# Performance work log

Measured on AMD Instinct MI355X. Metric: run time of the kernel, lower is better.

## Reference

```python
import jax, jax.numpy as jnp
import numpy as np

EPS = 1e-12
N = 8192
D_LOW = 2


def setup_inputs() -> dict:
    key = jax.random.key(0)
    k1, k2 = jax.random.split(key)
    # High-dim affinity distribution: strictly positive, sums to 1 (t-SNE P matrix)
    u = jax.random.uniform(k1, (N, N), dtype=jnp.float32, minval=0.1, maxval=1.0)
    P = u / u.sum()
    # Learned low-dim embedding (nn.Embedding(n, d).weight)
    Y = jax.random.normal(k2, (N, D_LOW), dtype=jnp.float32)
    dof = 1  # Student-t degrees of freedom (standard t-SNE)
    return {"P": P, "Y": Y, "dof": dof}


def reference(P, Y, dof):
    # Pairwise squared Euclidean distances: D[i,j] = ||Y_i - Y_j||^2
    Y2 = jnp.sum(Y * Y, axis=1, keepdims=True)          # (n, 1)
    Dm = Y2 - 2.0 * (Y @ Y.T) + Y2.T                     # (n, n)
    # Student-t affinities with zeroed diagonal
    Q = (1.0 + Dm / dof) ** (-(dof + 1) / 2.0)
    Q = Q.at[jnp.diag_indices(Q.shape[0])].set(0.0)
    # Global normalization + clamp
    Q = jnp.clip(Q / jnp.sum(Q), EPS)
    # KL(P || Q)  (metric == 'kl' branch)
    return jnp.sum(P * jnp.log(P / Q))
```

## Files before the change

kernel.cpp:

```cpp
#include <hip/hip_runtime.h>


static constexpr int NROWS = 8192;

__global__ __launch_bounds__(256) void kl_partial_kernel(
    const float* __restrict__ P, const float* __restrict__ Y,
    double* __restrict__ ws)
{
    const int nquads = (NROWS / 4) * NROWS;
    int tid = blockIdx.x * blockDim.x + threadIdx.x;
    int stride = gridDim.x * blockDim.x;

    const float4* __restrict__ P4 = reinterpret_cast<const float4*>(P);
    const float4* __restrict__ Y4 = reinterpret_cast<const float4*>(Y);
    const float2* __restrict__ Y2 = reinterpret_cast<const float2*>(Y);
    const float LOG_EPS = -27.63102111592855f;

    double sA = 0.0, sB = 0.0, sS = 0.0, sC = 0.0;

    for (int f = tid; f < nquads; f += stride) {
        int i  = f >> 11;
        int jq = f & 2047;
        int j0 = jq << 2;

        float4 p  = P4[f];
        float2 yi = Y2[i];
        float4 ya = Y4[jq << 1];
        float4 yb = Y4[(jq << 1) + 1];

        float pv[4]  = {p.x,  p.y,  p.z,  p.w};
        float yjx[4] = {ya.x, ya.z, yb.x, yb.z};
        float yjy[4] = {ya.y, ya.w, yb.y, yb.w};

#pragma unroll
        for (int k = 0; k < 4; ++k) {
            float dx  = yi.x - yjx[k];
            float dy  = yi.y - yjy[k];
            float opd = 1.0f + (dx * dx + dy * dy);
            if ((j0 + k) == i) {
                sC += (double)(pv[k] * (__logf(pv[k]) - LOG_EPS));
            } else {
                sS += (double)(1.0f / opd);
                sA += (double)(pv[k] * __logf(pv[k] * opd));
                sB += (double)pv[k];
            }
        }
    }

#pragma unroll
    for (int off = 32; off > 0; off >>= 1) {
        sA += __shfl_down(sA, off);
        sB += __shfl_down(sB, off);
        sS += __shfl_down(sS, off);
        sC += __shfl_down(sC, off);
    }

    __shared__ double red[4][4];
    int wave = threadIdx.x >> 6;
    int lane = threadIdx.x & 63;
    if (lane == 0) {
        red[wave][0] = sA; red[wave][1] = sB;
        red[wave][2] = sS; red[wave][3] = sC;
    }
    __syncthreads();
    if (threadIdx.x == 0) {
        double a = 0.0, b = 0.0, s = 0.0, c = 0.0;
#pragma unroll
        for (int w = 0; w < 4; ++w) {
            a += red[w][0]; b += red[w][1]; s += red[w][2]; c += red[w][3];
        }
        atomicAdd(&ws[0], a);
        atomicAdd(&ws[1], b);
        atomicAdd(&ws[2], s);
        atomicAdd(&ws[3], c);
    }
}

__global__ void kl_final_kernel(const double* __restrict__ ws,
                                float* __restrict__ out)
{
    double A = ws[0], B = ws[1], S = ws[2], C = ws[3];
    out[0] = (float)(A + B * log(S) + C);
}

extern "C" void kernel_launch(void* const* d_in, const int* in_sizes, int n_in,
                              void* d_out, int out_size, void* d_ws, size_t ws_size,
                              hipStream_t stream) {
    const float* P = (const float*)d_in[0];
    const float* Y = (const float*)d_in[1];
    double* ws = (double*)d_ws;

    hipMemsetAsync(d_ws, 0, 4 * sizeof(double), stream);

    dim3 grid(2048), block(256);
    hipLaunchKernelGGL(kl_partial_kernel, grid, block, 0, stream, P, Y, ws);
    hipLaunchKernelGGL(kl_final_kernel, dim3(1), dim3(1), 0, stream,
                       ws, (float*)d_out);
}
```

Measured before the change: 432.1 us.

## Map one block per row, use float accumulators, correct diagonal in final kernel

New measurement: 589.9 us. 36.5% more time.

```diff
diff --git a/kernel.cpp b/kernel.cpp
--- a/kernel.cpp
+++ b/kernel.cpp
@@ -1,86 +1,105 @@
 #include <hip/hip_runtime.h>
 
 
-static constexpr int NROWS = 8192;
+static constexpr int N_PTS = 8192;
+static constexpr int TPB   = 256;
+static constexpr int QPR   = N_PTS / 4;
+static constexpr int ITER  = QPR / TPB;
 
-__global__ __launch_bounds__(256) void kl_partial_kernel(
+__global__ __launch_bounds__(TPB) void kl_partial_kernel(
     const float* __restrict__ P, const float* __restrict__ Y,
     double* __restrict__ ws)
 {
-    const int nquads = (NROWS / 4) * NROWS;
-    int tid = blockIdx.x * blockDim.x + threadIdx.x;
-    int stride = gridDim.x * blockDim.x;
+    const int row = blockIdx.x;
+    const int t   = threadIdx.x;
+    const float4* __restrict__ P4 =
+        reinterpret_cast<const float4*>(P) + (size_t)row * QPR;
+    const float4* __restrict__ Y4 = reinterpret_cast<const float4*>(Y);
 
-    const float4* __restrict__ P4 = reinterpret_cast<const float4*>(P);
-    const float4* __restrict__ Y4 = reinterpret_cast<const float4*>(Y);
-    const float2* __restrict__ Y2 = reinterpret_cast<const float2*>(Y);
-    const float LOG_EPS = -27.63102111592855f;
+    const float yix = Y[2 * row];
+    const float yiy = Y[2 * row + 1];
 
-    double sA = 0.0, sB = 0.0, sS = 0.0, sC = 0.0;
+    float sA0 = 0.f, sA1 = 0.f, sB0 = 0.f, sB1 = 0.f, sS0 = 0.f, sS1 = 0.f;
 
-    for (int f = tid; f < nquads; f += stride) {
-        int i  = f >> 11;
-        int jq = f & 2047;
-        int j0 = jq << 2;
+#pragma unroll
+    for (int it = 0; it < ITER; ++it) {
+        const int jq = t + it * TPB;
+        float4 p  = P4[jq];
+        float4 ya = Y4[2 * jq];
+        float4 yb = Y4[2 * jq + 1];
 
-        float4 p  = P4[f];
-        float2 yi = Y2[i];
-        float4 ya = Y4[jq << 1];
-        float4 yb = Y4[(jq << 1) + 1];
-
-        float pv[4]  = {p.x,  p.y,  p.z,  p.w};
-        float yjx[4] = {ya.x, ya.z, yb.x, yb.z};
-        float yjy[4] = {ya.y, ya.w, yb.y, yb.w};
+        float pv[4] = {p.x,  p.y,  p.z,  p.w};
+        float jx[4] = {ya.x, ya.z, yb.x, yb.z};
+        float jy[4] = {ya.y, ya.w, yb.y, yb.w};
 
 #pragma unroll
         for (int k = 0; k < 4; ++k) {
-            float dx  = yi.x - yjx[k];
-            float dy  = yi.y - yjy[k];
-            float opd = 1.0f + (dx * dx + dy * dy);
-            if ((j0 + k) == i) {
-                sC += (double)(pv[k] * (__logf(pv[k]) - LOG_EPS));
+            float dx  = yix - jx[k];
+            float dy  = yiy - jy[k];
+            float opd = __builtin_fmaf(dy, dy, __builtin_fmaf(dx, dx, 1.0f));
+            float l   = __logf(pv[k] * opd);
+            float r   = __builtin_amdgcn_rcpf(opd);
+            if (k & 1) {
+                sA1 = __builtin_fmaf(pv[k], l, sA1);
+                sS1 += r;
+                sB1 += pv[k];
             } else {
-                sS += (double)(1.0f / opd);
-                sA += (double)(pv[k] * __logf(pv[k] * opd));
-                sB += (double)pv[k];
+                sA0 = __builtin_fmaf(pv[k], l, sA0);
+                sS0 += r;
+                sB0 += pv[k];
             }
         }
     }
 
+    double dA = (double)sA0 + (double)sA1;
+    double dB = (double)sB0 + (double)sB1;
+    double dS = (double)sS0 + (double)sS1;
+
 #pragma unroll
     for (int off = 32; off > 0; off >>= 1) {
-        sA += __shfl_down(sA, off);
-        sB += __shfl_down(sB, off);
-        sS += __shfl_down(sS, off);
-        sC += __shfl_down(sC, off);
+        dA += __shfl_down(dA, off);
+        dB += __shfl_down(dB, off);
+        dS += __shfl_down(dS, off);
     }
 
-    __shared__ double red[4][4];
-    int wave = threadIdx.x >> 6;
-    int lane = threadIdx.x & 63;
-    if (lane == 0) {
-        red[wave][0] = sA; red[wave][1] = sB;
-        red[wave][2] = sS; red[wave][3] = sC;
-    }
+    __shared__ double red[4][3];
+    const int wave = t >> 6, lane = t & 63;
+    if (lane == 0) { red[wave][0] = dA; red[wave][1] = dB; red[wave][2] = dS; }
     __syncthreads();
-    if (threadIdx.x == 0) {
-        double a = 0.0, b = 0.0, s = 0.0, c = 0.0;
-#pragma unroll
-        for (int w = 0; w < 4; ++w) {
-            a += red[w][0]; b += red[w][1]; s += red[w][2]; c += red[w][3];
-        }
+    if (t == 0) {
+        double a = red[0][0] + red[1][0] + red[2][0] + red[3][0];
+        double b = red[0][1] + red[1][1] + red[2][1] + red[3][1];
+        double s = red[0][2] + red[1][2] + red[2][2] + red[3][2];
         atomicAdd(&ws[0], a);
         atomicAdd(&ws[1], b);
         atomicAdd(&ws[2], s);
-        atomicAdd(&ws[3], c);
     }
 }
 
-__global__ void kl_final_kernel(const double* __restrict__ ws,
-                                float* __restrict__ out)
+__global__ __launch_bounds__(TPB) void kl_final_kernel(
+    const float* __restrict__ P, const double* __restrict__ ws,
+    float* __restrict__ out)
 {
-    double A = ws[0], B = ws[1], S = ws[2], C = ws[3];
-    out[0] = (float)(A + B * log(S) + C);
+    const int t = threadIdx.x;
+    double tr = 0.0;
+    for (int i = t; i < N_PTS; i += TPB)
+        tr += (double)P[(size_t)i * (N_PTS + 1)];
+
+#pragma unroll
+    for (int off = 32; off > 0; off >>= 1)
+        tr += __shfl_down(tr, off);
+
+    __shared__ double red[4];
+    if ((t & 63) == 0) red[t >> 6] = tr;
+    __syncthreads();
+    if (t == 0) {
+        double trace = red[0] + red[1] + red[2] + red[3];
+        double A = ws[0], B = ws[1], S = ws[2];
+        const double LOG_EPS = -27.631021115928547;
+        double kl = A + (B - trace) * log(S - (double)N_PTS)
+                      - trace * LOG_EPS;
+        out[0] = (float)kl;
+    }
 }
 
 extern "C" void kernel_launch(void* const* d_in, const int* in_sizes, int n_in,
@@ -90,10 +109,10 @@
     const float* Y = (const float*)d_in[1];
     double* ws = (double*)d_ws;
 
-    hipMemsetAsync(d_ws, 0, 4 * sizeof(double), stream);
+    hipMemsetAsync(d_ws, 0, 3 * sizeof(double), stream);
 
-    dim3 grid(2048), block(256);
-    hipLaunchKernelGGL(kl_partial_kernel, grid, block, 0, stream, P, Y, ws);
-    hipLaunchKernelGGL(kl_final_kernel, dim3(1), dim3(1), 0, stream,
-                       ws, (float*)d_out);
+    hipLaunchKernelGGL(kl_partial_kernel, dim3(N_PTS), dim3(TPB), 0, stream,
+                       P, Y, ws);
+    hipLaunchKernelGGL(kl_final_kernel, dim3(1), dim3(TPB), 0, stream,
+                       P, ws, (float*)d_out);
 }
```
